# Performance work log

Hardware: AMD Instinct MI355X
Metric: run time of the kernel (lower is better)

The kernel has to match this reference:

```python
import jax, jax.numpy as jnp
import numpy as np

SEQ_LEN = 512
DIM = 256
HEADS = 8
DIM_HEAD = 32
INNER = HEADS * DIM_HEAD
BATCH = 1
LN_EPS = 1e-5


def setup_inputs() -> dict:
    key = jax.random.key(0)
    ks = jax.random.split(key, 6)
    # kaiming_uniform_(a=sqrt(5)) on [L, in, out] -> bound = 1/sqrt(fan_in) with fan_in = in_dim*out_dim? 
    # torch computes fan_in from dims [1:] => fan_in = in_dim (dim of -2) * ... in practice bound ~ sqrt(1/fan_in);
    # exact init distribution is irrelevant for correctness testing, use uniform(+-1/sqrt(DIM)).
    s = 1.0 / np.sqrt(DIM)
    so = 1.0 / np.sqrt(INNER)
    return {
        "x": jax.random.normal(ks[0], (BATCH, SEQ_LEN, DIM), jnp.float32),
        "Wq": jax.random.uniform(ks[1], (SEQ_LEN, DIM, INNER), jnp.float32, -s, s),
        "Wk": jax.random.uniform(ks[2], (SEQ_LEN, DIM, INNER), jnp.float32, -s, s),
        "Wv": jax.random.uniform(ks[3], (SEQ_LEN, DIM, INNER), jnp.float32, -s, s),
        "gamma": jnp.ones((DIM,), jnp.float32),
        "beta": jnp.zeros((DIM,), jnp.float32),
        "Wo": jax.random.uniform(ks[4], (INNER, DIM), jnp.float32, -so, so),
        "bo": jnp.zeros((DIM,), jnp.float32),
    }


def reference(x, Wq, Wk, Wv, gamma, beta, Wo, bo):
    b, n, dim = x.shape
    h, dh = HEADS, DIM_HEAD
    # LayerNorm
    mu = jnp.mean(x, axis=-1, keepdims=True)
    var = jnp.mean((x - mu) ** 2, axis=-1, keepdims=True)
    xn = (x - mu) / jnp.sqrt(var + LN_EPS) * gamma + beta
    # Per-relative-index projections: pd[b, r, m, e] = xn[b, m] @ W[r]
    qd = jnp.einsum('bmc,rce->brme', xn, Wq)
    kd = jnp.einsum('bmc,rce->brme', xn, Wk)
    vd = jnp.einsum('bmc,rce->brme', xn, Wv)
    i = jnp.arange(n)
    # to_q / to_v index map: max(0, i - j); to_k (after rearrange swap) uses min(0, m - n) + n - 1
    rq = jnp.maximum(0, i[:, None] - i[None, :])          # [n(query), m(key)]
    rk = jnp.minimum(0, i[None, :] - i[:, None]) + n - 1  # [n, m]
    # q[b,n,m,e] = qd[b, rq[n,m], m]; k[b,n,m,e] = kd[b, rk[n,m], n]; v like q
    q_full = qd[:, rq, i[None, :], :].reshape(b, n, n, h, dh)
    k_full = kd[:, rk, i[:, None], :].reshape(b, n, n, h, dh)
    v_full = vd[:, rq, i[None, :], :].reshape(b, n, n, h, dh)
    scale = dh ** -0.5
    dots = jnp.einsum('bnmhd,bnmhd->bhnm', q_full, k_full) * scale
    causal = i[:, None] >= i[None, :]  # tril
    dots = jnp.where(causal[None, None], dots, -jnp.inf)
    attn = jax.nn.softmax(dots, axis=-1)
    out = jnp.einsum('bhnm,bnmhd->bnhd', attn, v_full).reshape(b, n, h * dh)
    return out @ Wo + bo
```

## Files before the change

kernel.cpp:

```cpp
#include <hip/hip_runtime.h>
#include <hip/hip_bf16.h>

typedef unsigned short u16;
typedef unsigned int   u32;
typedef __bf16 bf16x8 __attribute__((ext_vector_type(8)));
typedef float  f32x4  __attribute__((ext_vector_type(4)));
typedef u32    u32x4  __attribute__((ext_vector_type(4)));
typedef u32    u32x2  __attribute__((ext_vector_type(2)));

#define TRI_TOTAL 131328

__device__ __forceinline__ float b2f(u16 u) {
    return __builtin_bit_cast(float, ((u32)u) << 16);
}
__device__ __forceinline__ u16 f2b(float f) {
    return __builtin_bit_cast(u16, __float2bfloat16(f));
}
__device__ __forceinline__ int pcol(int col) {
    return (((col & 7) ^ ((col >> 3) & 7)) << 4);
}
__device__ __forceinline__ void gload_lds16(const void* g, void* l) {
    __builtin_amdgcn_global_load_lds(
        (const __attribute__((address_space(1))) void*)g,
        (__attribute__((address_space(3))) void*)l, 16, 0, 0);
}
__device__ __forceinline__ u32 qoff(int d) {
    return 512u * (u32)d - (u32)((d * (d - 1)) >> 1);
}
__device__ __forceinline__ u32 koff(int r) {
    return (u32)((r * (r + 1)) >> 1);
}

__global__ void __launch_bounds__(256) ln_kernel(const float* __restrict__ x,
                                                 const float* __restrict__ g,
                                                 const float* __restrict__ b,
                                                 u16* __restrict__ xn) {
    int n = blockIdx.x, t = threadIdx.x;
    float v = x[n * 256 + t];
    __shared__ float red[4];
    float s = v;
    #pragma unroll
    for (int o = 32; o >= 1; o >>= 1) s += __shfl_xor(s, o);
    if ((t & 63) == 0) red[t >> 6] = s;
    __syncthreads();
    float mu = (red[0] + red[1] + red[2] + red[3]) * (1.0f / 256.0f);
    float d = v - mu;
    __syncthreads();
    float s2 = d * d;
    #pragma unroll
    for (int o = 32; o >= 1; o >>= 1) s2 += __shfl_xor(s2, o);
    if ((t & 63) == 0) red[t >> 6] = s2;
    __syncthreads();
    float var = (red[0] + red[1] + red[2] + red[3]) * (1.0f / 256.0f);
    float y = d * rsqrtf(var + 1e-5f) * g[t] + b[t];
    xn[n * 256 + t] = f2b(y);
}

__global__ void __launch_bounds__(256) proj_kernel(
        const u16* __restrict__ xn,
        const float* __restrict__ Wq, const float* __restrict__ Wk,
        const float* __restrict__ Wv,
        u16* __restrict__ Qa, u16* __restrict__ Ka, u16* __restrict__ Va) {
    __shared__ char lds[65536 + 64 * 144];
    char* bufA = lds;
    char* bufB = lds + 32768;
    char* obuf = lds + 65536;

    int bid = blockIdx.x;
    int which = bid % 3;
    int rr = bid / 3;
    int strip = rr >> 2;
    int cs = rr & 3;
    const float* W = (which == 0) ? Wq : ((which == 1) ? Wk : Wv);
    u16* Out       = (which == 0) ? Qa : ((which == 1) ? Ka : Va);

    int t = threadIdx.x;
    int c0 = cs * 64;
    int wv  = t >> 6;
    int rg  = wv >> 1;
    int cg  = wv & 1;
    int L   = t & 63;
    int l15 = L & 15, l4 = L >> 4;
    int c4 = (t & 15) * 4;
    int kq = t >> 4;

    int r, rows, pbase;
    u32 obase;
#define SET_R(Q) do {                                                         \
    int rq_ = strip * 4 + (Q);                                                \
    r = (which == 1) ? (511 - rq_) : rq_;                                     \
    rows  = (which == 1) ? (r + 1) : (512 - r);                               \
    pbase = (which == 1) ? (511 - r) : 0;                                     \
    obase = (which == 1) ? koff(r) : qoff(r);                                 \
} while (0)
    SET_R(0);

#define DMA_TILE(DST, M0) do {                                                \
    _Pragma("unroll")                                                         \
    for (int j = 0; j < 8; ++j) {                                             \
        int lrow = wv * 16 + 2 * j + (L >> 5);                                \
        int grow = pbase + (M0) + lrow; if (grow > 511) grow = 511;           \
        const char* gp = (const char*)xn + (size_t)grow * 512                 \
                         + (((L & 31) ^ (lrow & 7)) << 4);                    \
        char* lp = (DST) + (wv * 16 + 2 * j) * 512;                           \
        gload_lds16(gp, lp);                                                  \
    }                                                                         \
} while (0)

#define DMA_WHALF(DST, R) do {                                                \
    const char* wsrc = (const char*)(W + ((size_t)(R) << 16) + c0);           \
    _Pragma("unroll")                                                         \
    for (int p = 0; p < 8; ++p) {                                             \
        int kk = p * 16 + (t >> 4);                                           \
        const char* gp = wsrc + (size_t)kk * 1024 + (t & 15) * 16;            \
        char* lp = (DST) + p * 4096 + (t >> 6) * 1024;                        \
        gload_lds16(gp, lp);                                                  \
    }                                                                         \
} while (0)

#define WLW(DST, IT, VA, VB, VC, VD) {                                        \
        int kbase2 = (kq * 4 + (IT) * 64) * 2;                                \
        _Pragma("unroll")                                                     \
        for (int i = 0; i < 4; ++i) {                                         \
            int col = c4 + i;                                                 \
            u32 lo = (u32)f2b(VA[i]) | ((u32)f2b(VB[i]) << 16);               \
            u32 hi = (u32)f2b(VC[i]) | ((u32)f2b(VD[i]) << 16);               \
            u32x2 pr; pr[0] = lo; pr[1] = hi;                                 \
            *(u32x2*)((DST) + col * 512 + (kbase2 ^ pcol(col))) = pr;         \
        }                                                                     \
    }

    DMA_TILE(bufB, 0);

    {
        const float* wp = W + ((size_t)r << 16) + c0 + c4 + (size_t)(kq * 4) * 256;
        f32x4 w00 = *(const f32x4*)(wp + 0);
        f32x4 w01 = *(const f32x4*)(wp + 256);
        f32x4 w02 = *(const f32x4*)(wp + 512);
        f32x4 w03 = *(const f32x4*)(wp + 768);
        f32x4 w10 = *(const f32x4*)(wp + 16384 + 0);
        f32x4 w11 = *(const f32x4*)(wp + 16384 + 256);
        f32x4 w12 = *(const f32x4*)(wp + 16384 + 512);
        f32x4 w13 = *(const f32x4*)(wp + 16384 + 768);
        f32x4 w20 = *(const f32x4*)(wp + 32768 + 0);
        f32x4 w21 = *(const f32x4*)(wp + 32768 + 256);
        f32x4 w22 = *(const f32x4*)(wp + 32768 + 512);
        f32x4 w23 = *(const f32x4*)(wp + 32768 + 768);
        f32x4 w30 = *(const f32x4*)(wp + 49152 + 0);
        f32x4 w31 = *(const f32x4*)(wp + 49152 + 256);
        f32x4 w32 = *(const f32x4*)(wp + 49152 + 512);
        f32x4 w33 = *(const f32x4*)(wp + 49152 + 768);
        WLW(bufA, 0, w00, w01, w02, w03)
        WLW(bufA, 1, w10, w11, w12, w13)
        WLW(bufA, 2, w20, w21, w22, w23)
        WLW(bufA, 3, w30, w31, w32, w33)
    }
    __syncthreads();

    bf16x8 b00, b01, b02, b03, b04, b05, b06, b07;
    bf16x8 b10, b11, b12, b13, b14, b15, b16, b17;
#define BEXT(SRC) do {                                                        \
    int colA_ = cg * 32 + l15, colB_ = cg * 32 + 16 + l15;                    \
    b00 = *(const bf16x8*)((SRC) + colA_ * 512 + ((0*64 + l4*16) ^ pcol(colA_))); \
    b01 = *(const bf16x8*)((SRC) + colA_ * 512 + ((1*64 + l4*16) ^ pcol(colA_))); \
    b02 = *(const bf16x8*)((SRC) + colA_ * 512 + ((2*64 + l4*16) ^ pcol(colA_))); \
    b03 = *(const bf16x8*)((SRC) + colA_ * 512 + ((3*64 + l4*16) ^ pcol(colA_))); \
    b04 = *(const bf16x8*)((SRC) + colA_ * 512 + ((4*64 + l4*16) ^ pcol(colA_))); \
    b05 = *(const bf16x8*)((SRC) + colA_ * 512 + ((5*64 + l4*16) ^ pcol(colA_))); \
    b06 = *(const bf16x8*)((SRC) + colA_ * 512 + ((6*64 + l4*16) ^ pcol(colA_))); \
    b07 = *(const bf16x8*)((SRC) + colA_ * 512 + ((7*64 + l4*16) ^ pcol(colA_))); \
    b10 = *(const bf16x8*)((SRC) + colB_ * 512 + ((0*64 + l4*16) ^ pcol(colB_))); \
    b11 = *(const bf16x8*)((SRC) + colB_ * 512 + ((1*64 + l4*16) ^ pcol(colB_))); \
    b12 = *(const bf16x8*)((SRC) + colB_ * 512 + ((2*64 + l4*16) ^ pcol(colB_))); \
    b13 = *(const bf16x8*)((SRC) + colB_ * 512 + ((3*64 + l4*16) ^ pcol(colB_))); \
    b14 = *(const bf16x8*)((SRC) + colB_ * 512 + ((4*64 + l4*16) ^ pcol(colB_))); \
    b15 = *(const bf16x8*)((SRC) + colB_ * 512 + ((5*64 + l4*16) ^ pcol(colB_))); \
    b16 = *(const bf16x8*)((SRC) + colB_ * 512 + ((6*64 + l4*16) ^ pcol(colB_))); \
    b17 = *(const bf16x8*)((SRC) + colB_ * 512 + ((7*64 + l4*16) ^ pcol(colB_))); \
} while (0)
    BEXT(bufA);
    __syncthreads();

    int am = (l15 & 7) << 4;
    char* cur = bufB;
    char* alt = bufA;
    int tr = t >> 2, qd = t & 3;

    for (int q = 0;;) {
        int rnext = 0;
        if (q < 3) { int rq_ = strip * 4 + q + 1;
                     rnext = (which == 1) ? (511 - rq_) : rq_; }
        int nt = (rows + 63) >> 6;
        for (int i = 0; i < nt; ++i) {
            int m0 = i << 6;
            bool lastt = (i + 1 >= nt);
            if (!lastt)          DMA_TILE(alt, m0 + 64);
            else if (q < 3)      DMA_WHALF(alt, rnext);

            const char* abase = cur + (rg * 32 + l15) * 512;
            f32x4 acc00 = {}, acc01 = {}, acc10 = {}, acc11 = {};
#define KS(ks) {                                                              \
        int kb = (ks) * 64 + l4 * 16;                                         \
        bf16x8 a0 = *(const bf16x8*)(abase + (kb ^ am));                      \
        bf16x8 a1 = *(const bf16x8*)(abase + 16 * 512 + (kb ^ am));           \
        acc00 = __builtin_amdgcn_mfma_f32_16x16x32_bf16(a0, b0##ks, acc00, 0, 0, 0); \
        acc01 = __builtin_amdgcn_mfma_f32_16x16x32_bf16(a0, b1##ks, acc01, 0, 0, 0); \
        acc10 = __builtin_amdgcn_mfma_f32_16x16x32_bf16(a1, b0##ks, acc10, 0, 0, 0); \
        acc11 = __builtin_amdgcn_mfma_f32_16x16x32_bf16(a1, b1##ks, acc11, 0, 0, 0); \
    }
            KS(0) KS(1) KS(2) KS(3) KS(4) KS(5) KS(6) KS(7)
#undef KS
            {
                char* ob = obuf + (size_t)(rg * 32) * 144 + (cg * 32 + l15) * 2;
                #pragma unroll
                for (int rf = 0; rf < 2; ++rf) {
                    f32x4 va = rf ? acc10 : acc00;
                    f32x4 vb = rf ? acc11 : acc01;
                    #pragma unroll
                    for (int j = 0; j < 4; ++j) {
                        int rl = rf * 16 + l4 * 4 + j;
                        *(u16*)(ob + rl * 144)      = f2b(va[j]);
                        *(u16*)(ob + rl * 144 + 32) = f2b(vb[j]);
                    }
                }
            }
            __syncthreads();
            {
                int ml = m0 + tr;
                if (ml < rows) {
                    u16* op = Out + (size_t)(obase + (u32)ml) * 256 + c0 + qd * 16;
                    const char* lb = obuf + tr * 144 + qd * 32;
                    u32x4 o0 = *(const u32x4*)(lb);
                    u32x4 o1 = *(const u32x4*)(lb + 16);
                    *(u32x4*)op = o0;
                    *(u32x4*)(op + 8) = o1;
                }
            }
            if (!lastt) { asm volatile("s_waitcnt vmcnt(2)" ::: "memory"); }
            else        { asm volatile("s_waitcnt vmcnt(0)" ::: "memory"); }
            __builtin_amdgcn_s_barrier();
            __builtin_amdgcn_sched_barrier(0);
            { char* tmp = cur; cur = alt; alt = tmp; }
        }
        if (++q > 3) break;
        SET_R(q);
        DMA_TILE(alt, 0);
        const float* wpg = W + ((size_t)r << 16) + c0 + c4;
        f32x4 gw0 = *(const f32x4*)(wpg + 32768 + (size_t)(kq * 4 + 0) * 256);
        f32x4 gw1 = *(const f32x4*)(wpg + 32768 + (size_t)(kq * 4 + 1) * 256);
        f32x4 gw2 = *(const f32x4*)(wpg + 32768 + (size_t)(kq * 4 + 2) * 256);
        f32x4 gw3 = *(const f32x4*)(wpg + 32768 + (size_t)(kq * 4 + 3) * 256);
        f32x4 gw4 = *(const f32x4*)(wpg + 49152 + (size_t)(kq * 4 + 0) * 256);
        f32x4 gw5 = *(const f32x4*)(wpg + 49152 + (size_t)(kq * 4 + 1) * 256);
        f32x4 gw6 = *(const f32x4*)(wpg + 49152 + (size_t)(kq * 4 + 2) * 256);
        f32x4 gw7 = *(const f32x4*)(wpg + 49152 + (size_t)(kq * 4 + 3) * 256);
        f32x4 lw0 = *(const f32x4*)(cur + (kq * 4 + 0) * 256 + (t & 15) * 16);
        f32x4 lw1 = *(const f32x4*)(cur + (kq * 4 + 1) * 256 + (t & 15) * 16);
        f32x4 lw2 = *(const f32x4*)(cur + (kq * 4 + 2) * 256 + (t & 15) * 16);
        f32x4 lw3 = *(const f32x4*)(cur + (kq * 4 + 3) * 256 + (t & 15) * 16);
        f32x4 lw4 = *(const f32x4*)(cur + (64 + kq * 4 + 0) * 256 + (t & 15) * 16);
        f32x4 lw5 = *(const f32x4*)(cur + (64 + kq * 4 + 1) * 256 + (t & 15) * 16);
        f32x4 lw6 = *(const f32x4*)(cur + (64 + kq * 4 + 2) * 256 + (t & 15) * 16);
        f32x4 lw7 = *(const f32x4*)(cur + (64 + kq * 4 + 3) * 256 + (t & 15) * 16);
        __syncthreads();
        WLW(cur, 0, lw0, lw1, lw2, lw3)
        WLW(cur, 1, lw4, lw5, lw6, lw7)
        WLW(cur, 2, gw0, gw1, gw2, gw3)
        WLW(cur, 3, gw4, gw5, gw6, gw7)
        asm volatile("s_waitcnt vmcnt(0)" ::: "memory");
        __syncthreads();
        BEXT(cur);
        __syncthreads();
        { char* tmp = cur; cur = alt; alt = tmp; }
    }
#undef DMA_TILE
#undef DMA_WHALF
#undef WLW
#undef BEXT
#undef SET_R
}

__global__ void __launch_bounds__(256) attn_kernel(const u16* __restrict__ Qa,
                                                   const u16* __restrict__ Ka,
                                                   const u16* __restrict__ Va,
                                                   float* __restrict__ ao) {
    int n = 511 - blockIdx.x, t = threadIdx.x;
    __shared__ float pbuf[512 * 9];
    __shared__ float linv[8];
    __shared__ u32 qrt[512];
    __shared__ u32 krt[512];
    int band = n + 1;

    for (int m = t; m < band; m += 256) {
        int dd = n - m;
        qrt[m] = qoff(dd) + (u32)m;
        krt[m] = koff(511 - dd) + (u32)m;
    }
    __syncthreads();

    int h = t & 7, mi = t >> 3;
    for (int m0 = 0; m0 < band; m0 += 32) {
        int m = m0 + mi;
        float d = -1e30f;
        if (m < band) {
            const char* qp = (const char*)Qa + (size_t)qrt[m] * 512 + h * 64;
            const char* kp = (const char*)Ka + (size_t)krt[m] * 512 + h * 64;
            float acc = 0.f;
            #pragma unroll
            for (int cch = 0; cch < 4; ++cch) {
                u32x4 qv = *reinterpret_cast<const u32x4*>(qp + cch * 16);
                u32x4 kv = *reinterpret_cast<const u32x4*>(kp + cch * 16);
                #pragma unroll
                for (int i = 0; i < 4; ++i) {
                    float ql = __builtin_bit_cast(float, qv[i] << 16);
                    float qh = __builtin_bit_cast(float, qv[i] & 0xffff0000u);
                    float kl = __builtin_bit_cast(float, kv[i] << 16);
                    float kh = __builtin_bit_cast(float, kv[i] & 0xffff0000u);
                    acc += ql * kl + qh * kh;
                }
            }
            d = acc * 0.17677669529663687f;
        }
        pbuf[m * 9 + h] = d;
    }
    __syncthreads();

    int wv = t >> 6, L = t & 63;
    for (int s = 0; s < 2; ++s) {
        int hh = wv + s * 4;
        float mx = -1e30f;
        for (int m = L; m < band; m += 64) mx = fmaxf(mx, pbuf[m * 9 + hh]);
        #pragma unroll
        for (int o = 32; o >= 1; o >>= 1) mx = fmaxf(mx, __shfl_xor(mx, o));
        float sum = 0.f;
        for (int m = L; m < band; m += 64) {
            float p = __expf(pbuf[m * 9 + hh] - mx);
            pbuf[m * 9 + hh] = p;
            sum += p;
        }
        #pragma unroll
        for (int o = 32; o >= 1; o >>= 1) sum += __shfl_xor(sum, o);
        if (L == 0) linv[hh] = 1.0f / sum;
    }
    __syncthreads();

    int h2 = t >> 5;
    const char* vb = (const char*)Va + (size_t)t * 2;
    const float* pb = pbuf + h2;
    float a0 = 0, a1 = 0, a2 = 0, a3 = 0, a4 = 0, a5 = 0, a6 = 0, a7 = 0;
    int m = 0;
#define VROW(MM) ((size_t)qrt[MM] * 512)
    for (; m + 16 <= band; m += 16) {
        u16 v0  = *(const u16*)(vb + VROW(m +  0));
        u16 v1  = *(const u16*)(vb + VROW(m +  1));
        u16 v2  = *(const u16*)(vb + VROW(m +  2));
        u16 v3  = *(const u16*)(vb + VROW(m +  3));
        u16 v4  = *(const u16*)(vb + VROW(m +  4));
        u16 v5  = *(const u16*)(vb + VROW(m +  5));
        u16 v6  = *(const u16*)(vb + VROW(m +  6));
        u16 v7  = *(const u16*)(vb + VROW(m +  7));
        u16 v8  = *(const u16*)(vb + VROW(m +  8));
        u16 v9  = *(const u16*)(vb + VROW(m +  9));
        u16 v10 = *(const u16*)(vb + VROW(m + 10));
        u16 v11 = *(const u16*)(vb + VROW(m + 11));
        u16 v12 = *(const u16*)(vb + VROW(m + 12));
        u16 v13 = *(const u16*)(vb + VROW(m + 13));
        u16 v14 = *(const u16*)(vb + VROW(m + 14));
        u16 v15 = *(const u16*)(vb + VROW(m + 15));
        a0 += pb[(m +  0) * 9] * b2f(v0);
        a1 += pb[(m +  1) * 9] * b2f(v1);
        a2 += pb[(m +  2) * 9] * b2f(v2);
        a3 += pb[(m +  3) * 9] * b2f(v3);
        a4 += pb[(m +  4) * 9] * b2f(v4);
        a5 += pb[(m +  5) * 9] * b2f(v5);
        a6 += pb[(m +  6) * 9] * b2f(v6);
        a7 += pb[(m +  7) * 9] * b2f(v7);
        a0 += pb[(m +  8) * 9] * b2f(v8);
        a1 += pb[(m +  9) * 9] * b2f(v9);
        a2 += pb[(m + 10) * 9] * b2f(v10);
        a3 += pb[(m + 11) * 9] * b2f(v11);
        a4 += pb[(m + 12) * 9] * b2f(v12);
        a5 += pb[(m + 13) * 9] * b2f(v13);
        a6 += pb[(m + 14) * 9] * b2f(v14);
        a7 += pb[(m + 15) * 9] * b2f(v15);
    }
    for (; m < band; ++m)
        a0 += pb[m * 9] * b2f(*(const u16*)(vb + VROW(m)));
#undef VROW
    ao[n * 256 + t] = (((a0 + a1) + (a2 + a3)) + ((a4 + a5) + (a6 + a7)))
                      * linv[h2];
}

__global__ void __launch_bounds__(256) outproj_kernel(const float* __restrict__ ao,
                                                      const float* __restrict__ Wo,
                                                      const float* __restrict__ bo,
                                                      float* __restrict__ out) {
    int n = blockIdx.x, e = threadIdx.x;
    const float* a = ao + n * 256;
    float c0 = bo[e], c1 = 0, c2 = 0, c3 = 0;
    for (int c = 0; c < 256; c += 4) {
        c0 += a[c + 0] * Wo[(c + 0) * 256 + e];
        c1 += a[c + 1] * Wo[(c + 1) * 256 + e];
        c2 += a[c + 2] * Wo[(c + 2) * 256 + e];
        c3 += a[c + 3] * Wo[(c + 3) * 256 + e];
    }
    out[n * 256 + e] = (c0 + c1) + (c2 + c3);
}

extern "C" void kernel_launch(void* const* d_in, const int* in_sizes, int n_in,
                              void* d_out, int out_size, void* d_ws, size_t ws_size,
                              hipStream_t stream) {
    const float* x     = (const float*)d_in[0];
    const float* Wq    = (const float*)d_in[1];
    const float* Wk    = (const float*)d_in[2];
    const float* Wv    = (const float*)d_in[3];
    const float* gamma = (const float*)d_in[4];
    const float* beta  = (const float*)d_in[5];
    const float* Wo    = (const float*)d_in[6];
    const float* bo    = (const float*)d_in[7];
    float* out = (float*)d_out;

    char* ws = (char*)d_ws;
    u16* xn = (u16*)ws;
    size_t off = (size_t)512 * 256 * 2;
    u16* Qa = (u16*)(ws + off); off += (size_t)TRI_TOTAL * 256 * 2;
    u16* Ka = (u16*)(ws + off); off += (size_t)TRI_TOTAL * 256 * 2;
    u16* Va = (u16*)(ws + off); off += (size_t)TRI_TOTAL * 256 * 2;
    float* ao = (float*)(ws + off);

    ln_kernel<<<512, 256, 0, stream>>>(x, gamma, beta, xn);
    proj_kernel<<<1536, 256, 0, stream>>>(xn, Wq, Wk, Wv, Qa, Ka, Va);
    attn_kernel<<<512, 256, 0, stream>>>(Qa, Ka, Va, ao);
    outproj_kernel<<<512, 256, 0, stream>>>(ao, Wo, bo, out);
}
```

Before: 228.3 us.

## Shrink projection kernel LDS footprint with 32-row tiles and half-K weight staging

The projection kernel's LDS drops from about 73 KB to about 37 KB. It uses 32-row xn tiles, each wave computes one 16-row fragment, and the bf16-converted weight slab is staged through LDS in two K halves instead of one full 64 KB buffer. The aim is to raise occupancy so more blocks fit per CU and hide memory latency. In exchange, the pipelined prefetch of the next r's weights during the last tile is removed, weight loading is now serialized at the start of each r with extra barriers, and each tile does half the MFMA work per sync.

```diff
diff --git a/kernel.cpp b/kernel.cpp
--- a/kernel.cpp
+++ b/kernel.cpp
@@ -6,7 +6,6 @@
 typedef __bf16 bf16x8 __attribute__((ext_vector_type(8)));
 typedef float  f32x4  __attribute__((ext_vector_type(4)));
 typedef u32    u32x4  __attribute__((ext_vector_type(4)));
-typedef u32    u32x2  __attribute__((ext_vector_type(2)));
 
 #define TRI_TOTAL 131328
 
@@ -61,10 +60,8 @@
         const float* __restrict__ Wq, const float* __restrict__ Wk,
         const float* __restrict__ Wv,
         u16* __restrict__ Qa, u16* __restrict__ Ka, u16* __restrict__ Va) {
-    __shared__ char lds[65536 + 64 * 144];
-    char* bufA = lds;
-    char* bufB = lds + 32768;
-    char* obuf = lds + 65536;
+    __shared__ char lds[16384 * 2 + 32 * 144];
+    char* obuf = lds + 32768;
 
     int bid = blockIdx.x;
     int which = bid % 3;
@@ -93,190 +90,129 @@
     pbase = (which == 1) ? (511 - r) : 0;                                     \
     obase = (which == 1) ? koff(r) : qoff(r);                                 \
 } while (0)
-    SET_R(0);
 
 #define DMA_TILE(DST, M0) do {                                                \
     _Pragma("unroll")                                                         \
-    for (int j = 0; j < 8; ++j) {                                             \
-        int lrow = wv * 16 + 2 * j + (L >> 5);                                \
+    for (int j = 0; j < 4; ++j) {                                             \
+        int lrow = wv * 8 + 2 * j + (L >> 5);                                 \
         int grow = pbase + (M0) + lrow; if (grow > 511) grow = 511;           \
         const char* gp = (const char*)xn + (size_t)grow * 512                 \
                          + (((L & 31) ^ (lrow & 7)) << 4);                    \
-        char* lp = (DST) + (wv * 16 + 2 * j) * 512;                           \
+        char* lp = (DST) + (wv * 8 + 2 * j) * 512;                            \
         gload_lds16(gp, lp);                                                  \
     }                                                                         \
 } while (0)
 
-#define DMA_WHALF(DST, R) do {                                                \
-    const char* wsrc = (const char*)(W + ((size_t)(R) << 16) + c0);           \
+#define W_HALF(DST, K0) do {                                                  \
+    const float* wp_ = W + ((size_t)r << 16) + c0 + c4                        \
+                       + (size_t)((K0) + kq * 8) * 256;                       \
+    f32x4 h0 = *(const f32x4*)(wp_ + 0 * 256);                                \
+    f32x4 h1 = *(const f32x4*)(wp_ + 1 * 256);                                \
+    f32x4 h2 = *(const f32x4*)(wp_ + 2 * 256);                                \
+    f32x4 h3 = *(const f32x4*)(wp_ + 3 * 256);                                \
+    f32x4 h4 = *(const f32x4*)(wp_ + 4 * 256);                                \
+    f32x4 h5 = *(const f32x4*)(wp_ + 5 * 256);                                \
+    f32x4 h6 = *(const f32x4*)(wp_ + 6 * 256);                                \
+    f32x4 h7 = *(const f32x4*)(wp_ + 7 * 256);                                \
     _Pragma("unroll")                                                         \
-    for (int p = 0; p < 8; ++p) {                                             \
-        int kk = p * 16 + (t >> 4);                                           \
-        const char* gp = wsrc + (size_t)kk * 1024 + (t & 15) * 16;            \
-        char* lp = (DST) + p * 4096 + (t >> 6) * 1024;                        \
-        gload_lds16(gp, lp);                                                  \
+    for (int c = 0; c < 4; ++c) {                                             \
+        int col = c4 + c;                                                     \
+        u32x4 pr;                                                             \
+        pr[0] = (u32)f2b(h0[c]) | ((u32)f2b(h1[c]) << 16);                    \
+        pr[1] = (u32)f2b(h2[c]) | ((u32)f2b(h3[c]) << 16);                    \
+        pr[2] = (u32)f2b(h4[c]) | ((u32)f2b(h5[c]) << 16);                    \
+        pr[3] = (u32)f2b(h6[c]) | ((u32)f2b(h7[c]) << 16);                    \
+        *(u32x4*)((DST) + col * 256 + ((kq * 16) ^ pcol(col))) = pr;          \
     }                                                                         \
 } while (0)
-
-#define WLW(DST, IT, VA, VB, VC, VD) {                                        \
-        int kbase2 = (kq * 4 + (IT) * 64) * 2;                                \
-        _Pragma("unroll")                                                     \
-        for (int i = 0; i < 4; ++i) {                                         \
-            int col = c4 + i;                                                 \
-            u32 lo = (u32)f2b(VA[i]) | ((u32)f2b(VB[i]) << 16);               \
-            u32 hi = (u32)f2b(VC[i]) | ((u32)f2b(VD[i]) << 16);               \
-            u32x2 pr; pr[0] = lo; pr[1] = hi;                                 \
-            *(u32x2*)((DST) + col * 512 + (kbase2 ^ pcol(col))) = pr;         \
-        }                                                                     \
-    }
-
-    DMA_TILE(bufB, 0);
-
-    {
-        const float* wp = W + ((size_t)r << 16) + c0 + c4 + (size_t)(kq * 4) * 256;
-        f32x4 w00 = *(const f32x4*)(wp + 0);
-        f32x4 w01 = *(const f32x4*)(wp + 256);
-        f32x4 w02 = *(const f32x4*)(wp + 512);
-        f32x4 w03 = *(const f32x4*)(wp + 768);
-        f32x4 w10 = *(const f32x4*)(wp + 16384 + 0);
-        f32x4 w11 = *(const f32x4*)(wp + 16384 + 256);
-        f32x4 w12 = *(const f32x4*)(wp + 16384 + 512);
-        f32x4 w13 = *(const f32x4*)(wp + 16384 + 768);
-        f32x4 w20 = *(const f32x4*)(wp + 32768 + 0);
-        f32x4 w21 = *(const f32x4*)(wp + 32768 + 256);
-        f32x4 w22 = *(const f32x4*)(wp + 32768 + 512);
-        f32x4 w23 = *(const f32x4*)(wp + 32768 + 768);
-        f32x4 w30 = *(const f32x4*)(wp + 49152 + 0);
-        f32x4 w31 = *(const f32x4*)(wp + 49152 + 256);
-        f32x4 w32 = *(const f32x4*)(wp + 49152 + 512);
-        f32x4 w33 = *(const f32x4*)(wp + 49152 + 768);
-        WLW(bufA, 0, w00, w01, w02, w03)
-        WLW(bufA, 1, w10, w11, w12, w13)
-        WLW(bufA, 2, w20, w21, w22, w23)
-        WLW(bufA, 3, w30, w31, w32, w33)
-    }
-    __syncthreads();
 
     bf16x8 b00, b01, b02, b03, b04, b05, b06, b07;
     bf16x8 b10, b11, b12, b13, b14, b15, b16, b17;
-#define BEXT(SRC) do {                                                        \
-    int colA_ = cg * 32 + l15, colB_ = cg * 32 + 16 + l15;                    \
-    b00 = *(const bf16x8*)((SRC) + colA_ * 512 + ((0*64 + l4*16) ^ pcol(colA_))); \
-    b01 = *(const bf16x8*)((SRC) + colA_ * 512 + ((1*64 + l4*16) ^ pcol(colA_))); \
-    b02 = *(const bf16x8*)((SRC) + colA_ * 512 + ((2*64 + l4*16) ^ pcol(colA_))); \
-    b03 = *(const bf16x8*)((SRC) + colA_ * 512 + ((3*64 + l4*16) ^ pcol(colA_))); \
-    b04 = *(const bf16x8*)((SRC) + colA_ * 512 + ((4*64 + l4*16) ^ pcol(colA_))); \
-    b05 = *(const bf16x8*)((SRC) + colA_ * 512 + ((5*64 + l4*16) ^ pcol(colA_))); \
-    b06 = *(const bf16x8*)((SRC) + colA_ * 512 + ((6*64 + l4*16) ^ pcol(colA_))); \
-    b07 = *(const bf16x8*)((SRC) + colA_ * 512 + ((7*64 + l4*16) ^ pcol(colA_))); \
-    b10 = *(const bf16x8*)((SRC) + colB_ * 512 + ((0*64 + l4*16) ^ pcol(colB_))); \
-    b11 = *(const bf16x8*)((SRC) + colB_ * 512 + ((1*64 + l4*16) ^ pcol(colB_))); \
-    b12 = *(const bf16x8*)((SRC) + colB_ * 512 + ((2*64 + l4*16) ^ pcol(colB_))); \
-    b13 = *(const bf16x8*)((SRC) + colB_ * 512 + ((3*64 + l4*16) ^ pcol(colB_))); \
-    b14 = *(const bf16x8*)((SRC) + colB_ * 512 + ((4*64 + l4*16) ^ pcol(colB_))); \
-    b15 = *(const bf16x8*)((SRC) + colB_ * 512 + ((5*64 + l4*16) ^ pcol(colB_))); \
-    b16 = *(const bf16x8*)((SRC) + colB_ * 512 + ((6*64 + l4*16) ^ pcol(colB_))); \
-    b17 = *(const bf16x8*)((SRC) + colB_ * 512 + ((7*64 + l4*16) ^ pcol(colB_))); \
-} while (0)
-    BEXT(bufA);
-    __syncthreads();
+    int colA = cg * 32 + l15, colB = cg * 32 + 16 + l15;
+    int pA = pcol(colA), pB = pcol(colB);
+#define BEXT_H0(SRC) do {                                                     \
+    b00 = *(const bf16x8*)((SRC) + colA * 256 + ((0 * 64 + l4 * 16) ^ pA));   \
+    b01 = *(const bf16x8*)((SRC) + colA * 256 + ((1 * 64 + l4 * 16) ^ pA));   \
+    b02 = *(const bf16x8*)((SRC) + colA * 256 + ((2 * 64 + l4 * 16) ^ pA));   \
+    b03 = *(const bf16x8*)((SRC) + colA * 256 + ((3 * 64 + l4 * 16) ^ pA));   \
+    b10 = *(const bf16x8*)((SRC) + colB * 256 + ((0 * 64 + l4 * 16) ^ pB));   \
+    b11 = *(const bf16x8*)((SRC) + colB * 256 + ((1 * 64 + l4 * 16) ^ pB));   \
+    b12 = *(const bf16x8*)((SRC) + colB * 256 + ((2 * 64 + l4 * 16) ^ pB));   \
+    b13 = *(const bf16x8*)((SRC) + colB * 256 + ((3 * 64 + l4 * 16) ^ pB));   \
+} while (0)
+#define BEXT_H1(SRC) do {                                                     \
+    b04 = *(const bf16x8*)((SRC) + colA * 256 + ((0 * 64 + l4 * 16) ^ pA));   \
+    b05 = *(const bf16x8*)((SRC) + colA * 256 + ((1 * 64 + l4 * 16) ^ pA));   \
+    b06 = *(const bf16x8*)((SRC) + colA * 256 + ((2 * 64 + l4 * 16) ^ pA));   \
+    b07 = *(const bf16x8*)((SRC) + colA * 256 + ((3 * 64 + l4 * 16) ^ pA));   \
+    b14 = *(const bf16x8*)((SRC) + colB * 256 + ((0 * 64 + l4 * 16) ^ pB));   \
+    b15 = *(const bf16x8*)((SRC) + colB * 256 + ((1 * 64 + l4 * 16) ^ pB));   \
+    b16 = *(const bf16x8*)((SRC) + colB * 256 + ((2 * 64 + l4 * 16) ^ pB));   \
+    b17 = *(const bf16x8*)((SRC) + colB * 256 + ((3 * 64 + l4 * 16) ^ pB));   \
+} while (0)
 
     int am = (l15 & 7) << 4;
-    char* cur = bufB;
-    char* alt = bufA;
-    int tr = t >> 2, qd = t & 3;
-
-    for (int q = 0;;) {
-        int rnext = 0;
-        if (q < 3) { int rq_ = strip * 4 + q + 1;
-                     rnext = (which == 1) ? (511 - rq_) : rq_; }
-        int nt = (rows + 63) >> 6;
+    char* cur = lds;
+    char* alt = lds + 16384;
+    int tr2 = t >> 3, sg = t & 7;
+
+    for (int q = 0; q < 4; ++q) {
+        SET_R(q);
+        DMA_TILE(cur, 0);
+        W_HALF(alt, 0);
+        __syncthreads();
+        BEXT_H0(alt);
+        __syncthreads();
+        W_HALF(alt, 128);
+        __syncthreads();
+        BEXT_H1(alt);
+        asm volatile("s_waitcnt vmcnt(0)" ::: "memory");
+        __syncthreads();
+
+        int nt = (rows + 31) >> 5;
         for (int i = 0; i < nt; ++i) {
-            int m0 = i << 6;
+            int m0 = i << 5;
             bool lastt = (i + 1 >= nt);
-            if (!lastt)          DMA_TILE(alt, m0 + 64);
-            else if (q < 3)      DMA_WHALF(alt, rnext);
-
-            const char* abase = cur + (rg * 32 + l15) * 512;
-            f32x4 acc00 = {}, acc01 = {}, acc10 = {}, acc11 = {};
+            if (!lastt) DMA_TILE(alt, m0 + 32);
+
+            const char* abase = cur + (rg * 16 + l15) * 512;
+            f32x4 acc0 = {}, acc1 = {};
 #define KS(ks) {                                                              \
         int kb = (ks) * 64 + l4 * 16;                                         \
         bf16x8 a0 = *(const bf16x8*)(abase + (kb ^ am));                      \
-        bf16x8 a1 = *(const bf16x8*)(abase + 16 * 512 + (kb ^ am));           \
-        acc00 = __builtin_amdgcn_mfma_f32_16x16x32_bf16(a0, b0##ks, acc00, 0, 0, 0); \
-        acc01 = __builtin_amdgcn_mfma_f32_16x16x32_bf16(a0, b1##ks, acc01, 0, 0, 0); \
-        acc10 = __builtin_amdgcn_mfma_f32_16x16x32_bf16(a1, b0##ks, acc10, 0, 0, 0); \
-        acc11 = __builtin_amdgcn_mfma_f32_16x16x32_bf16(a1, b1##ks, acc11, 0, 0, 0); \
+        acc0 = __builtin_amdgcn_mfma_f32_16x16x32_bf16(a0, b0##ks, acc0, 0, 0, 0); \
+        acc1 = __builtin_amdgcn_mfma_f32_16x16x32_bf16(a0, b1##ks, acc1, 0, 0, 0); \
     }
             KS(0) KS(1) KS(2) KS(3) KS(4) KS(5) KS(6) KS(7)
 #undef KS
             {
-                char* ob = obuf + (size_t)(rg * 32) * 144 + (cg * 32 + l15) * 2;
+                char* ob = obuf + (size_t)(rg * 16) * 144 + (cg * 32 + l15) * 2;
                 #pragma unroll
-                for (int rf = 0; rf < 2; ++rf) {
-                    f32x4 va = rf ? acc10 : acc00;
-                    f32x4 vb = rf ? acc11 : acc01;
-                    #pragma unroll
-                    for (int j = 0; j < 4; ++j) {
-                        int rl = rf * 16 + l4 * 4 + j;
-                        *(u16*)(ob + rl * 144)      = f2b(va[j]);
-                        *(u16*)(ob + rl * 144 + 32) = f2b(vb[j]);
-                    }
+                for (int j = 0; j < 4; ++j) {
+                    int rl = l4 * 4 + j;
+                    *(u16*)(ob + rl * 144)      = f2b(acc0[j]);
+                    *(u16*)(ob + rl * 144 + 32) = f2b(acc1[j]);
                 }
             }
             __syncthreads();
             {
-                int ml = m0 + tr;
+                int ml = m0 + tr2;
                 if (ml < rows) {
-                    u16* op = Out + (size_t)(obase + (u32)ml) * 256 + c0 + qd * 16;
-                    const char* lb = obuf + tr * 144 + qd * 32;
-                    u32x4 o0 = *(const u32x4*)(lb);
-                    u32x4 o1 = *(const u32x4*)(lb + 16);
-                    *(u32x4*)op = o0;
-                    *(u32x4*)(op + 8) = o1;
+                    u16* op = Out + (size_t)(obase + (u32)ml) * 256 + c0 + sg * 8;
+                    *(u32x4*)op = *(const u32x4*)(obuf + tr2 * 144 + sg * 16);
                 }
             }
-            if (!lastt) { asm volatile("s_waitcnt vmcnt(2)" ::: "memory"); }
+            if (!lastt) { asm volatile("s_waitcnt vmcnt(1)" ::: "memory"); }
             else        { asm volatile("s_waitcnt vmcnt(0)" ::: "memory"); }
             __builtin_amdgcn_s_barrier();
             __builtin_amdgcn_sched_barrier(0);
             { char* tmp = cur; cur = alt; alt = tmp; }
         }
-        if (++q > 3) break;
-        SET_R(q);
-        DMA_TILE(alt, 0);
-        const float* wpg = W + ((size_t)r << 16) + c0 + c4;
-        f32x4 gw0 = *(const f32x4*)(wpg + 32768 + (size_t)(kq * 4 + 0) * 256);
-        f32x4 gw1 = *(const f32x4*)(wpg + 32768 + (size_t)(kq * 4 + 1) * 256);
-        f32x4 gw2 = *(const f32x4*)(wpg + 32768 + (size_t)(kq * 4 + 2) * 256);
-        f32x4 gw3 = *(const f32x4*)(wpg + 32768 + (size_t)(kq * 4 + 3) * 256);
-        f32x4 gw4 = *(const f32x4*)(wpg + 49152 + (size_t)(kq * 4 + 0) * 256);
-        f32x4 gw5 = *(const f32x4*)(wpg + 49152 + (size_t)(kq * 4 + 1) * 256);
-        f32x4 gw6 = *(const f32x4*)(wpg + 49152 + (size_t)(kq * 4 + 2) * 256);
-        f32x4 gw7 = *(const f32x4*)(wpg + 49152 + (size_t)(kq * 4 + 3) * 256);
-        f32x4 lw0 = *(const f32x4*)(cur + (kq * 4 + 0) * 256 + (t & 15) * 16);
-        f32x4 lw1 = *(const f32x4*)(cur + (kq * 4 + 1) * 256 + (t & 15) * 16);
-        f32x4 lw2 = *(const f32x4*)(cur + (kq * 4 + 2) * 256 + (t & 15) * 16);
-        f32x4 lw3 = *(const f32x4*)(cur + (kq * 4 + 3) * 256 + (t & 15) * 16);
-        f32x4 lw4 = *(const f32x4*)(cur + (64 + kq * 4 + 0) * 256 + (t & 15) * 16);
-        f32x4 lw5 = *(const f32x4*)(cur + (64 + kq * 4 + 1) * 256 + (t & 15) * 16);
-        f32x4 lw6 = *(const f32x4*)(cur + (64 + kq * 4 + 2) * 256 + (t & 15) * 16);
-        f32x4 lw7 = *(const f32x4*)(cur + (64 + kq * 4 + 3) * 256 + (t & 15) * 16);
-        __syncthreads();
-        WLW(cur, 0, lw0, lw1, lw2, lw3)
-        WLW(cur, 1, lw4, lw5, lw6, lw7)
-        WLW(cur, 2, gw0, gw1, gw2, gw3)
-        WLW(cur, 3, gw4, gw5, gw6, gw7)
-        asm volatile("s_waitcnt vmcnt(0)" ::: "memory");
-        __syncthreads();
-        BEXT(cur);
-        __syncthreads();
-        { char* tmp = cur; cur = alt; alt = tmp; }
     }
 #undef DMA_TILE
-#undef DMA_WHALF
-#undef WLW
-#undef BEXT
+#undef W_HALF
+#undef BEXT_H0
+#undef BEXT_H1
 #undef SET_R
 }
 
```

Result: slower. 234.9 us (+2.9%).
